# Performance work log

Measured on AMD Instinct MI355X. Metric: run time of the kernel, lower is better.

## Reference

```python
import jax, jax.numpy as jnp
import numpy as np

B, C, H, W = 8, 256, 64, 64
CI = C // 2  # inter_channels


def setup_inputs() -> dict:
    key = jax.random.key(0)
    ks = jax.random.split(key, 9)
    s_in = 1.0 / np.sqrt(C)
    s_ci = 1.0 / np.sqrt(CI)
    return {
        "x": jax.random.normal(ks[0], (B, C, H, W), dtype=jnp.float32),
        "g_w": jax.random.uniform(ks[1], (CI, C), jnp.float32, -s_in, s_in),
        "g_b": jax.random.uniform(ks[2], (CI,), jnp.float32, -s_in, s_in),
        "theta_w": jax.random.uniform(ks[3], (CI, C), jnp.float32, -s_in, s_in),
        "theta_b": jax.random.uniform(ks[4], (CI,), jnp.float32, -s_in, s_in),
        "phi_w": jax.random.uniform(ks[5], (CI, C), jnp.float32, -s_in, s_in),
        "phi_b": jax.random.uniform(ks[6], (CI,), jnp.float32, -s_in, s_in),
        "W_w": jax.random.uniform(ks[7], (C, CI), jnp.float32, -s_ci, s_ci),
        "W_b": jax.random.uniform(ks[8], (C,), jnp.float32, -s_ci, s_ci),
    }


def reference(x, g_w, g_b, theta_w, theta_b, phi_w, phi_b, W_w, W_b):
    b, c, h, w = x.shape
    xf = x.reshape(b, c, h * w)  # [B, C, N]
    # 1x1 convs == per-pixel linear maps
    g_x = jnp.einsum("oc,bcn->bon", g_w, xf) + g_b[:, None]      # [B, CI, N]
    theta_x = jnp.einsum("oc,bcn->bon", theta_w, xf) + theta_b[:, None]
    phi_x = jnp.einsum("oc,bcn->bon", phi_w, xf) + phi_b[:, None]
    # attention_map[b, i, j] = <theta[:, i], phi[:, j]>, softmax over j
    attn = jax.nn.softmax(jnp.einsum("bci,bcj->bij", theta_x, phi_x), axis=-1)
    # y[b, c, i] = sum_j g_x[b, c, j] * attn[b, i, j]
    y = jnp.einsum("bcj,bij->bci", g_x, attn)  # [B, CI, N]
    out = jnp.einsum("oc,bcn->bon", W_w, y) + W_b[:, None]  # [B, C, N]
    return out.reshape(b, c, h, w) + x
```

## Files before the change

### kernel.cpp

```cpp
#include <hip/hip_runtime.h>
#include <hip/hip_bf16.h>

#define B_  8
#define C_  256
#define CI_ 128
#define N_  4096

typedef __bf16 bf16;
typedef __attribute__((ext_vector_type(8))) __bf16 bf16x8;
typedef __attribute__((ext_vector_type(4))) __bf16 bf16x4;
typedef __attribute__((ext_vector_type(4))) float  floatx4;

static_assert(sizeof(bf16) == 2, "bf16 size");

__device__ inline floatx4 mfma16(bf16x8 a, bf16x8 b, floatx4 c) {
    return __builtin_amdgcn_mfma_f32_16x16x32_bf16(a, b, c, 0, 0, 0);
}

__device__ inline bool detect_fp32(const void* probe) {
    const unsigned short* u = (const unsigned short*)probe;
    int lane = threadIdx.x & 63;
    unsigned short w = u[lane * 2];
    int ex = (w >> 7) & 0xFF;
    bool insane = !((ex > 96 && ex < 143) || (w & 0x7FFF) == 0);
    unsigned long long b = __ballot(insane);
    return __popcll(b) > 16;
}

__device__ inline bf16x8 load8(const void* p, size_t i, bool fp32) {
    if (!fp32) return *(const bf16x8*)((const bf16*)p + i);
    const float* f = (const float*)p + i;
    floatx4 a = *(const floatx4*)(f);
    floatx4 c = *(const floatx4*)(f + 4);
    bf16x8 r;
    r[0] = (bf16)a[0]; r[1] = (bf16)a[1]; r[2] = (bf16)a[2]; r[3] = (bf16)a[3];
    r[4] = (bf16)c[0]; r[5] = (bf16)c[1]; r[6] = (bf16)c[2]; r[7] = (bf16)c[3];
    return r;
}

__device__ inline float loadv(const void* p, size_t i, bool fp32) {
    return fp32 ? ((const float*)p)[i] : (float)((const bf16*)p)[i];
}

__device__ inline bf16x8 cvt8(floatx4 a, floatx4 b) {
    bf16x8 r;
    r[0] = (bf16)a[0]; r[1] = (bf16)a[1]; r[2] = (bf16)a[2]; r[3] = (bf16)a[3];
    r[4] = (bf16)b[0]; r[5] = (bf16)b[1]; r[6] = (bf16)b[2]; r[7] = (bf16)b[3];
    return r;
}

__global__ __launch_bounds__(512) void proj3_kernel(
    const void* __restrict__ x,
    const void* __restrict__ wt, const void* __restrict__ bt,
    const void* __restrict__ wp, const void* __restrict__ bp,
    const void* __restrict__ wg, const void* __restrict__ bg,
    bf16* __restrict__ T, bf16* __restrict__ P, bf16* __restrict__ G)
{
    const bool fp32 = detect_fp32(x);

    const int b  = blockIdx.y;
    const int n0 = blockIdx.x * 128;

    __shared__ bf16 xT[128][40];
    __shared__ bf16 wl[384][40];

    const int t    = threadIdx.x;
    const int w    = t >> 6;
    const int lane = t & 63;
    const int l15  = lane & 15;
    const int quad = lane >> 4;
    const int wm   = w >> 1;
    const int wn   = w & 1;

    const int sc = t >> 4;
    const int sm = t & 15;
    const int wr = t >> 2;
    const int wc = (t & 3) * 8;

    floatx4 acc[6][4];
#pragma unroll
    for (int f = 0; f < 6; ++f)
#pragma unroll
        for (int ni = 0; ni < 4; ++ni) acc[f][ni] = (floatx4)0.f;

    floatx4 pxa, pxb; bf16x8 pxh;
    floatx4 pwa[3], pwb[3]; bf16x8 pwh[3];

    auto issue = [&](int k) {
        size_t xo = ((size_t)b * C_ + k + sc) * N_ + n0 + sm * 8;
        if (fp32) {
            const float* fx_ = (const float*)x + xo;
            pxa = *(const floatx4*)fx_;
            pxb = *(const floatx4*)(fx_ + 4);
        } else {
            pxh = *(const bf16x8*)((const bf16*)x + xo);
        }
#pragma unroll
        for (int p = 0; p < 3; ++p) {
            const void* ws = (p == 0) ? wt : (p == 1) ? wp : wg;
            size_t wo = (size_t)wr * C_ + k + wc;
            if (fp32) {
                const float* fw_ = (const float*)ws + wo;
                pwa[p] = *(const floatx4*)fw_;
                pwb[p] = *(const floatx4*)(fw_ + 4);
            } else {
                pwh[p] = *(const bf16x8*)((const bf16*)ws + wo);
            }
        }
    };

    issue(0);

    for (int ks = 0; ks < 8; ++ks) {
        {
            bf16x8 xv = fp32 ? cvt8(pxa, pxb) : pxh;
            int colx = ((((sc >> 3) + sm) & 3) << 3) + (sc & 7);
#pragma unroll
            for (int i = 0; i < 8; ++i) xT[sm * 8 + i][colx] = xv[i];
#pragma unroll
            for (int p = 0; p < 3; ++p) {
                bf16x8 wv = fp32 ? cvt8(pwa[p], pwb[p]) : pwh[p];
                *(bf16x8*)(&wl[p * 128 + wr][wc]) = wv;
            }
        }
        __syncthreads();

        if (ks < 7) issue((ks + 1) * 32);

        bf16x8 fxr[4], fwr[6];
#pragma unroll
        for (int ni = 0; ni < 4; ++ni) {
            int px = wn * 64 + ni * 16 + l15;
            int ch = (quad + (px >> 3)) & 3;
            fxr[ni] = *(const bf16x8*)(&xT[px][ch * 8]);
        }
#pragma unroll
        for (int f = 0; f < 6; ++f)
            fwr[f] = *(const bf16x8*)(&wl[f * 64 + wm * 16 + l15][quad * 8]);

#pragma unroll
        for (int f = 0; f < 4; ++f)
#pragma unroll
            for (int ni = 0; ni < 4; ++ni)
                acc[f][ni] = mfma16(fxr[ni], fwr[f], acc[f][ni]);
#pragma unroll
        for (int f = 4; f < 6; ++f)
#pragma unroll
            for (int ni = 0; ni < 4; ++ni)
                acc[f][ni] = mfma16(fwr[f], fxr[ni], acc[f][ni]);

        __syncthreads();
    }

#pragma unroll
    for (int f = 0; f < 6; ++f) {
        const void* bsel = (f < 2) ? bt : (f < 4) ? bp : bg;
        if (f < 4) {
            bf16* outp = ((f < 2) ? T : P) + (size_t)b * N_ * CI_;
            int o = (f & 1) * 64 + wm * 16 + l15;
            float bv = loadv(bsel, o, fp32);
#pragma unroll
            for (int ni = 0; ni < 4; ++ni)
#pragma unroll
                for (int r = 0; r < 4; ++r) {
                    int px = n0 + wn * 64 + ni * 16 + quad * 4 + r;
                    outp[(size_t)px * CI_ + o] = (bf16)(acc[f][ni][r] + bv);
                }
        } else {
            bf16* outp = G + (size_t)b * CI_ * N_;
#pragma unroll
            for (int r = 0; r < 4; ++r) {
                int o = (f & 1) * 64 + wm * 16 + quad * 4 + r;
                float bv = loadv(bsel, o, fp32);
#pragma unroll
                for (int ni = 0; ni < 4; ++ni) {
                    int px = n0 + wn * 64 + ni * 16 + l15;
                    outp[(size_t)o * N_ + px] = (bf16)(acc[f][ni][r] + bv);
                }
            }
        }
    }
}

__global__ __launch_bounds__(512) void attn_kernel(
    const bf16* __restrict__ T,
    const bf16* __restrict__ P,
    const bf16* __restrict__ G,
    const void* __restrict__ Ww,
    const void* __restrict__ Wb,
    const void* __restrict__ x,
    void* __restrict__ out)
{
    const int bid = blockIdx.x;
    const int b   = bid & 7;
    const int i0  = (bid >> 3) * 128;

    __shared__ __align__(16) char smem[133120];

    const bool fp32 = detect_fp32(x);

    const int t    = threadIdx.x;
    const int w    = t >> 6;
    const int g    = w >> 2;
    const int wg   = w & 3;
    const int tg   = t & 255;
    const int lane = t & 63;
    const int l15  = lane & 15;
    const int quad = lane >> 4;
    const int m7   = l15 & 7;

    bf16* Kl = (bf16*)(smem + g * 32768);
    bf16* Vt = (bf16*)(smem + g * 32768 + 16384);
    bf16* Pw = (bf16*)(smem + 65536 + w * 4096);

    const bf16* Kb = P + (size_t)b * N_ * CI_;
    const bf16* Vb = G + (size_t)b * CI_ * N_;
    const int jbase = g * 2048;

    bf16x8 qf[2][4];
#pragma unroll
    for (int rf = 0; rf < 2; ++rf) {
        const bf16* Qb = T + ((size_t)b * N_ + i0 + wg * 32 + rf * 16 + l15) * CI_;
#pragma unroll
        for (int ks = 0; ks < 4; ++ks)
            qf[rf][ks] = *(const bf16x8*)(Qb + ks * 32 + quad * 8);
    }

    floatx4 O[2][8];
#pragma unroll
    for (int rf = 0; rf < 2; ++rf)
#pragma unroll
        for (int cf = 0; cf < 8; ++cf) O[rf][cf] = (floatx4)0.f;
    float lsum[2][4];
#pragma unroll
    for (int rf = 0; rf < 2; ++rf)
#pragma unroll
        for (int r = 0; r < 4; ++r) lsum[rf][r] = 0.f;

    bf16x8 kreg[4], vreg[4];
#pragma unroll
    for (int s = 0; s < 4; ++s) {
        int id = tg + s * 256;
        kreg[s] = *(const bf16x8*)(Kb + (size_t)(jbase + (id >> 4)) * CI_ + (id & 15) * 8);
        vreg[s] = *(const bf16x8*)(Vb + (size_t)(id >> 3) * N_ + jbase + (id & 7) * 8);
    }

    for (int it = 0; it < 32; ++it) {
#pragma unroll
        for (int s = 0; s < 4; ++s) {
            int id = tg + s * 256;
            int kr = id >> 4, kc = id & 15;
            int vr = id >> 3, vc = id & 7;
            *(bf16x8*)(Kl + kr * 128 + ((kc ^ (kr & 7)) * 8)) = kreg[s];
            *(bf16x8*)(Vt + vr * 64  + ((vc ^ (vr & 7)) * 8)) = vreg[s];
        }
        __syncthreads();

        if (it < 31) {
            int j0n = jbase + (it + 1) * 64;
#pragma unroll
            for (int s = 0; s < 4; ++s) {
                int id = tg + s * 256;
                kreg[s] = *(const bf16x8*)(Kb + (size_t)(j0n + (id >> 4)) * CI_ + (id & 15) * 8);
                vreg[s] = *(const bf16x8*)(Vb + (size_t)(id >> 3) * N_ + j0n + (id & 7) * 8);
            }
        }

        floatx4 S[2][4];
#pragma unroll
        for (int jf = 0; jf < 4; ++jf) {
            floatx4 s0 = (floatx4)0.f, s1 = (floatx4)0.f;
#pragma unroll
            for (int ks = 0; ks < 4; ++ks) {
                bf16x8 kf = *(const bf16x8*)(
                    Kl + (jf * 16 + l15) * 128 + (((ks * 4 + quad) ^ m7) * 8));
                s0 = mfma16(qf[0][ks], kf, s0);
                s1 = mfma16(qf[1][ks], kf, s1);
            }
            S[0][jf] = s0;
            S[1][jf] = s1;
        }

#pragma unroll
        for (int rf = 0; rf < 2; ++rf)
#pragma unroll
            for (int r = 0; r < 4; ++r) {
                float p0 = __expf(S[rf][0][r]);
                float p1 = __expf(S[rf][1][r]);
                float p2 = __expf(S[rf][2][r]);
                float p3 = __expf(S[rf][3][r]);
                lsum[rf][r] += (p0 + p1) + (p2 + p3);
                int row = rf * 16 + quad * 4 + r;
                int r7  = (quad * 4 + r) & 7;
                int cb  = l15 >> 3;
                int base = row * 64 + (l15 & 7);
                Pw[base + ((0 + cb) ^ r7) * 8] = (bf16)p0;
                Pw[base + ((2 + cb) ^ r7) * 8] = (bf16)p1;
                Pw[base + ((4 + cb) ^ r7) * 8] = (bf16)p2;
                Pw[base + ((6 + cb) ^ r7) * 8] = (bf16)p3;
            }

#pragma unroll
        for (int ks = 0; ks < 2; ++ks) {
            int cx = ((ks * 4 + quad) ^ m7) * 8;
            bf16x8 pf0 = *(const bf16x8*)(Pw + l15 * 64 + cx);
            bf16x8 pf1 = *(const bf16x8*)(Pw + (16 + l15) * 64 + cx);
#pragma unroll
            for (int cf = 0; cf < 8; ++cf) {
                bf16x8 vf = *(const bf16x8*)(Vt + (cf * 16 + l15) * 64 + cx);
                O[0][cf] = mfma16(pf0, vf, O[0][cf]);
                O[1][cf] = mfma16(pf1, vf, O[1][cf]);
            }
        }
        __syncthreads();
    }

    float* scrO = (float*)smem;
    float* scrL = (float*)(smem + 65536);
    bf16*  Yl   = (bf16*)(smem + 98304);
    if (g == 1) {
#pragma unroll
        for (int rf = 0; rf < 2; ++rf)
#pragma unroll
            for (int cf = 0; cf < 8; ++cf)
#pragma unroll
                for (int r = 0; r < 4; ++r)
                    scrO[(rf * 32 + cf * 4 + r) * 256 + wg * 64 + lane] = O[rf][cf][r];
#pragma unroll
        for (int rf = 0; rf < 2; ++rf)
#pragma unroll
            for (int r = 0; r < 4; ++r)
                scrL[(rf * 4 + r) * 256 + wg * 64 + lane] = lsum[rf][r];
    }
    __syncthreads();
    if (g == 0) {
#pragma unroll
        for (int rf = 0; rf < 2; ++rf)
#pragma unroll
            for (int cf = 0; cf < 8; ++cf)
#pragma unroll
                for (int r = 0; r < 4; ++r)
                    O[rf][cf][r] += scrO[(rf * 32 + cf * 4 + r) * 256 + wg * 64 + lane];

#pragma unroll
        for (int rf = 0; rf < 2; ++rf)
#pragma unroll
            for (int r = 0; r < 4; ++r) {
                float rs = lsum[rf][r] + scrL[(rf * 4 + r) * 256 + wg * 64 + lane];
                rs += __shfl_xor(rs, 1);
                rs += __shfl_xor(rs, 2);
                rs += __shfl_xor(rs, 4);
                rs += __shfl_xor(rs, 8);
                lsum[rf][r] = 1.f / rs;
            }

#pragma unroll
        for (int rf = 0; rf < 2; ++rf)
#pragma unroll
            for (int cf = 0; cf < 8; ++cf)
#pragma unroll
                for (int r = 0; r < 4; ++r) {
                    int px = wg * 32 + rf * 16 + quad * 4 + r;
                    Yl[px * 136 + cf * 16 + l15] =
                        (bf16)(O[rf][cf][r] * lsum[rf][r]);
                }
    }
    __syncthreads();

    bf16* Wl = (bf16*)smem;
#pragma unroll
    for (int p = 0; p < 16; ++p) {
        int idx = p * 2048 + t * 4;
        int o   = idx >> 7;
        int ci  = idx & 127;
        bf16x4 v;
        if (fp32) {
            floatx4 f4 = *(const floatx4*)((const float*)Ww + idx);
            v[0] = (bf16)f4[0]; v[1] = (bf16)f4[1];
            v[2] = (bf16)f4[2]; v[3] = (bf16)f4[3];
        } else {
            v = *(const bf16x4*)((const bf16*)Ww + idx);
        }
        *(bf16x4*)(&Wl[o * 136 + ci]) = v;
    }
    __syncthreads();

    {
        const int wm = w >> 1;
        const int wn = w & 1;
        floatx4 acc[4][4];
#pragma unroll
        for (int i = 0; i < 4; ++i)
#pragma unroll
            for (int j = 0; j < 4; ++j) acc[i][j] = (floatx4)0.f;

#pragma unroll
        for (int ks = 0; ks < 4; ++ks) {
            bf16x8 fa[4], fb[4];
#pragma unroll
            for (int i = 0; i < 4; ++i) {
                fa[i] = *(const bf16x8*)(&Wl[(wm * 64 + i * 16 + l15) * 136 + ks * 32 + quad * 8]);
                fb[i] = *(const bf16x8*)(&Yl[(wn * 64 + i * 16 + l15) * 136 + ks * 32 + quad * 8]);
            }
#pragma unroll
            for (int mi = 0; mi < 4; ++mi)
#pragma unroll
                for (int ni = 0; ni < 4; ++ni)
                    acc[mi][ni] = mfma16(fa[mi], fb[ni], acc[mi][ni]);
        }

#pragma unroll
        for (int mi = 0; mi < 4; ++mi)
#pragma unroll
            for (int ni = 0; ni < 4; ++ni)
#pragma unroll
                for (int r = 0; r < 4; ++r) {
                    int oo = wm * 64 + mi * 16 + quad * 4 + r;
                    int px = i0 + wn * 64 + ni * 16 + l15;
                    size_t idx = ((size_t)b * C_ + oo) * N_ + px;
                    float v = acc[mi][ni][r] + loadv(Wb, oo, fp32)
                            + loadv(x, idx, fp32);
                    if (fp32) ((float*)out)[idx] = v;
                    else      ((bf16*)out)[idx] = (bf16)v;
                }
    }
}

extern "C" void kernel_launch(void* const* d_in, const int* in_sizes, int n_in,
                              void* d_out, int out_size, void* d_ws, size_t ws_size,
                              hipStream_t stream) {
    const void* x    = d_in[0];
    const void* g_w  = d_in[1];
    const void* g_b  = d_in[2];
    const void* th_w = d_in[3];
    const void* th_b = d_in[4];
    const void* ph_w = d_in[5];
    const void* ph_b = d_in[6];
    const void* W_w  = d_in[7];
    const void* W_b  = d_in[8];

    const size_t plane = (size_t)B_ * N_ * CI_;
    bf16* T = (bf16*)d_ws;
    bf16* P = T + plane;
    bf16* G = P + plane;

    proj3_kernel<<<dim3(N_ / 128, B_), 512, 0, stream>>>(
        x, th_w, th_b, ph_w, ph_b, g_w, g_b, T, P, G);
    attn_kernel<<<dim3(N_ / 128 * B_), 512, 0, stream>>>(
        T, P, G, W_w, W_b, x, d_out);
}
```

Measured before the change: 215.2 us.

## Double-buffer K/V tiles in LDS to drop one barrier per iteration

K and V staging in shared memory now uses two buffers per group. The next tile is written into the alternate buffer after the MFMA work, so each loop iteration needs one barrier instead of two. LDS usage grows from 130 KB to 160 KB per block, which may limit occupancy (already one 512-thread block per CU). Epilogue scratch reuse now depends on the final barrier after the loop.

```diff
diff --git a/kernel.cpp b/kernel.cpp
--- a/kernel.cpp
+++ b/kernel.cpp
@@ -12,6 +12,8 @@
 typedef __attribute__((ext_vector_type(4))) float  floatx4;
 
 static_assert(sizeof(bf16) == 2, "bf16 size");
+
+#define KV_ELEMS 8192
 
 __device__ inline floatx4 mfma16(bf16x8 a, bf16x8 b, floatx4 c) {
     return __builtin_amdgcn_mfma_f32_16x16x32_bf16(a, b, c, 0, 0, 0);
@@ -195,7 +197,7 @@
     const int b   = bid & 7;
     const int i0  = (bid >> 3) * 128;
 
-    __shared__ __align__(16) char smem[133120];
+    __shared__ __align__(16) char smem[163840];
 
     const bool fp32 = detect_fp32(x);
 
@@ -209,9 +211,7 @@
     const int quad = lane >> 4;
     const int m7   = l15 & 7;
 
-    bf16* Kl = (bf16*)(smem + g * 32768);
-    bf16* Vt = (bf16*)(smem + g * 32768 + 16384);
-    bf16* Pw = (bf16*)(smem + 65536 + w * 4096);
+    bf16* Pw = (bf16*)(smem + 131072 + w * 4096);
 
     const bf16* Kb = P + (size_t)b * N_ * CI_;
     const bf16* Vb = G + (size_t)b * CI_ * N_;
@@ -245,15 +245,24 @@
         vreg[s] = *(const bf16x8*)(Vb + (size_t)(id >> 3) * N_ + jbase + (id & 7) * 8);
     }
 
-    for (int it = 0; it < 32; ++it) {
+    {
+        bf16* K0 = (bf16*)(smem + g * 65536);
+        bf16* V0 = K0 + KV_ELEMS;
 #pragma unroll
         for (int s = 0; s < 4; ++s) {
             int id = tg + s * 256;
-            int kr = id >> 4, kc = id & 15;
-            int vr = id >> 3, vc = id & 7;
-            *(bf16x8*)(Kl + kr * 128 + ((kc ^ (kr & 7)) * 8)) = kreg[s];
-            *(bf16x8*)(Vt + vr * 64  + ((vc ^ (vr & 7)) * 8)) = vreg[s];
-        }
+            int krr = id >> 4, kcc = id & 15;
+            int vrr = id >> 3, vcc = id & 7;
+            *(bf16x8*)(K0 + krr * 128 + ((kcc ^ (krr & 7)) * 8)) = kreg[s];
+            *(bf16x8*)(V0 + vrr * 64  + ((vcc ^ (vrr & 7)) * 8)) = vreg[s];
+        }
+    }
+
+    for (int it = 0; it < 32; ++it) {
+        const int cur = it & 1;
+        bf16* Kl = (bf16*)(smem + g * 65536 + cur * 32768);
+        bf16* Vt = Kl + KV_ELEMS;
+
         __syncthreads();
 
         if (it < 31) {
@@ -312,8 +321,21 @@
                 O[1][cf] = mfma16(pf1, vf, O[1][cf]);
             }
         }
-        __syncthreads();
-    }
+
+        if (it < 31) {
+            bf16* Kn = (bf16*)(smem + g * 65536 + (cur ^ 1) * 32768);
+            bf16* Vn = Kn + KV_ELEMS;
+#pragma unroll
+            for (int s = 0; s < 4; ++s) {
+                int id = tg + s * 256;
+                int krr = id >> 4, kcc = id & 15;
+                int vrr = id >> 3, vcc = id & 7;
+                *(bf16x8*)(Kn + krr * 128 + ((kcc ^ (krr & 7)) * 8)) = kreg[s];
+                *(bf16x8*)(Vn + vrr * 64  + ((vcc ^ (vrr & 7)) * 8)) = vreg[s];
+            }
+        }
+    }
+    __syncthreads();
 
     float* scrO = (float*)smem;
     float* scrL = (float*)(smem + 65536);
```

Measured after the change: 221.1 us. 2.7% more time.
